# Kernel optimization log

Measured on AMD Instinct MI355X. Metric: run time of the kernel, lower is better.

Reference implementation:

```python
import jax, jax.numpy as jnp
import numpy as np
import math

DIM_V = 512
NUM_HEADS = 8
LN_EPS = 1e-5


def _layer_norm(x, g, b):
    mu = jnp.mean(x, axis=-1, keepdims=True)
    var = jnp.mean(jnp.square(x - mu), axis=-1, keepdims=True)
    return (x - mu) * jax.lax.rsqrt(var + LN_EPS) * g + b


def setup_inputs() -> dict:
    key = jax.random.key(0)
    ks = jax.random.split(key, 12)
    B, Nq, Nk, Dq, Dk, Dv = 16, 1024, 1024, 512, 512, DIM_V
    s_q = 1.0 / math.sqrt(Dq)
    s_k = 1.0 / math.sqrt(Dk)
    s_v = 1.0 / math.sqrt(Dv)
    return {
        "Q": jax.random.normal(ks[0], (B, Nq, Dq), jnp.float32),
        "K": jax.random.normal(ks[1], (B, Nk, Dk), jnp.float32),
        "Wq": jax.random.normal(ks[2], (Dq, Dv), jnp.float32) * s_q,
        "bq": jnp.zeros((Dv,), jnp.float32),
        "Wk": jax.random.normal(ks[3], (Dk, Dv), jnp.float32) * s_k,
        "bk": jnp.zeros((Dv,), jnp.float32),
        "Wv": jax.random.normal(ks[4], (Dk, Dv), jnp.float32) * s_k,
        "bv": jnp.zeros((Dv,), jnp.float32),
        "Wo": jax.random.normal(ks[5], (Dv, Dv), jnp.float32) * s_v,
        "bo": jnp.zeros((Dv,), jnp.float32),
        "g0": jnp.ones((Dv,), jnp.float32),
        "b0": jnp.zeros((Dv,), jnp.float32),
        "g1": jnp.ones((Dv,), jnp.float32),
        "b1": jnp.zeros((Dv,), jnp.float32),
    }


def reference(Q, K, Wq, bq, Wk, bk, Wv, bv, Wo, bo, g0, b0, g1, b1):
    B, Nq, _ = Q.shape
    H = NUM_HEADS
    hd = DIM_V // H
    Qp = Q @ Wq + bq            # [B, Nq, Dv]
    Kp = K @ Wk + bk            # [B, Nk, Dv]
    Vp = K @ Wv + bv            # [B, Nk, Dv]
    # split heads: [B, N, H, hd]
    Qh = Qp.reshape(B, Nq, H, hd)
    Kh = Kp.reshape(B, -1, H, hd)
    Vh = Vp.reshape(B, -1, H, hd)
    # NOTE: original scales by sqrt(dim_V), not sqrt(head_dim)
    scores = jnp.einsum("bqhd,bkhd->bhqk", Qh, Kh) / math.sqrt(DIM_V)
    A = jax.nn.softmax(scores, axis=-1)          # [B, H, Nq, Nk]
    Oh = Qh + jnp.einsum("bhqk,bkhd->bqhd", A, Vh)  # residual on projected Q
    O = Oh.reshape(B, Nq, DIM_V)
    O = _layer_norm(O, g0, b0)
    O = O + jax.nn.relu(O @ Wo + bo)
    O = _layer_norm(O, g1, b1)
    return O
```

## Files before the change

### kernel.cpp

```cpp
#include <hip/hip_runtime.h>
#include <hip/hip_bf16.h>

typedef float f32x4 __attribute__((ext_vector_type(4)));
typedef float f32x16 __attribute__((ext_vector_type(16)));
typedef __bf16 bf16x8 __attribute__((ext_vector_type(8)));
typedef __bf16 bf16x4 __attribute__((ext_vector_type(4)));

#define MFMA(a, b, c) __builtin_amdgcn_mfma_f32_16x16x32_bf16(a, b, c, 0, 0, 0)
#define MFMA32(a, b, c) __builtin_amdgcn_mfma_f32_32x32x16_bf16(a, b, c, 0, 0, 0)
#define AS1 __attribute__((address_space(1)))
#define AS3 __attribute__((address_space(3)))

__device__ __forceinline__ void gload16(const void* g, void* l) {
    __builtin_amdgcn_global_load_lds((const AS1 unsigned int*)g, (AS3 unsigned int*)l, 16, 0, 0);
}

__device__ __forceinline__ unsigned short f2bf(float f) {
    union { float f; unsigned u; } x{f};
    unsigned r = x.u + 0x7FFFu + ((x.u >> 16) & 1u);
    return (unsigned short)(r >> 16);
}
__device__ __forceinline__ float bf2f(unsigned short u) {
    union { unsigned u; float f; } x; x.u = ((unsigned)u) << 16; return x.f;
}
__device__ __forceinline__ unsigned pkbf(float a, float b) {
    union { __bf16 h[2]; unsigned u; } r;
    r.h[0] = (__bf16)a; r.h[1] = (__bf16)b;
    return r.u;
}

__device__ __forceinline__ void softmax_pack(const f32x16& s0, const f32x16& s1,
                                             float& ls, int hi, bf16x8* pf) {
    unsigned We[8], Wf[8];
    #pragma unroll
    for (int g = 0; g < 4; ++g) {
        float e0 = __builtin_amdgcn_exp2f(s0[4 * g + 0]);
        float e1 = __builtin_amdgcn_exp2f(s0[4 * g + 1]);
        float e2 = __builtin_amdgcn_exp2f(s0[4 * g + 2]);
        float e3 = __builtin_amdgcn_exp2f(s0[4 * g + 3]);
        float f0 = __builtin_amdgcn_exp2f(s1[4 * g + 0]);
        float f1 = __builtin_amdgcn_exp2f(s1[4 * g + 1]);
        float f2 = __builtin_amdgcn_exp2f(s1[4 * g + 2]);
        float f3 = __builtin_amdgcn_exp2f(s1[4 * g + 3]);
        ls += ((e0 + e1) + (e2 + e3)) + ((f0 + f1) + (f2 + f3));
        We[2 * g + 0] = pkbf(e0, e1); We[2 * g + 1] = pkbf(e2, e3);
        Wf[2 * g + 0] = pkbf(f0, f1); Wf[2 * g + 1] = pkbf(f2, f3);
    }
    #pragma unroll
    for (int src = 0; src < 2; ++src) {
        const unsigned* W = src == 0 ? We : Wf;
        #pragma unroll
        for (int k2 = 0; k2 < 2; ++k2) {
            unsigned A0 = W[4 * k2 + 0], A1 = W[4 * k2 + 1];
            unsigned B0 = W[4 * k2 + 2], B1 = W[4 * k2 + 3];
            unsigned cross0 = __shfl_xor(hi ? A0 : B0, 32);
            unsigned cross1 = __shfl_xor(hi ? A1 : B1, 32);
            union { unsigned w[4]; bf16x8 v; } r;
            r.w[0] = hi ? cross0 : A0;
            r.w[1] = hi ? cross1 : A1;
            r.w[2] = hi ? B0 : cross0;
            r.w[3] = hi ? B1 : cross1;
            pf[src * 2 + k2] = r.v;
        }
    }
}

__global__ __launch_bounds__(256) void k_transpose4(const float* W0, const float* W1,
                                                    const float* W2, const float* W3,
                                                    unsigned short* T0, unsigned short* T1,
                                                    unsigned short* T2, unsigned short* T3) {
    __shared__ float T[64][65];
    int sel = blockIdx.x >> 6, tile = blockIdx.x & 63;
    const float* W = sel == 0 ? W0 : sel == 1 ? W1 : sel == 2 ? W2 : W3;
    unsigned short* Wt = sel == 0 ? T0 : sel == 1 ? T1 : sel == 2 ? T2 : T3;
    int k0 = (tile >> 3) * 64, n0 = (tile & 7) * 64;
    int tid = threadIdx.x;
    for (int it = 0; it < 16; ++it) {
        int id = it * 256 + tid;
        int r = id >> 6, c = id & 63;
        T[r][c] = W[(k0 + r) * 512 + n0 + c];
    }
    __syncthreads();
    for (int it = 0; it < 16; ++it) {
        int id = it * 256 + tid;
        int r = id >> 6, c = id & 63;
        Wt[(n0 + r) * 512 + k0 + c] = f2bf(T[c][r]);
    }
}

__global__ __launch_bounds__(256) void k_proj(const float* __restrict__ Qf,
                                              const float* __restrict__ Kf,
                                              const unsigned short* __restrict__ Wqt,
                                              const unsigned short* __restrict__ Wkt,
                                              const unsigned short* __restrict__ Wvt,
                                              const float* __restrict__ bq,
                                              const float* __restrict__ bk,
                                              const float* __restrict__ bv,
                                              unsigned short* __restrict__ Qsc,
                                              unsigned short* __restrict__ Kpo,
                                              unsigned short* __restrict__ VpT,
                                              float scale2) {
    __shared__ __align__(16) float AbS[2][4096];
    __shared__ __align__(16) unsigned short BbS[2][4096];
    const int tid = threadIdx.x;
    const int lane = tid & 63, w = tid >> 6;
    const int sel = blockIdx.x >> 9;
    int ib = blockIdx.x & 511;
    const float* A = sel == 0 ? Qf : Kf;
    const unsigned short* Bt = sel == 0 ? Wqt : sel == 1 ? Wkt : Wvt;
    const float* bias = sel == 0 ? bq : sel == 1 ? bk : bv;
    const float scale = sel == 0 ? scale2 : 1.0f;
    const int mt = (ib & 7) | ((ib >> 5) << 3), nt = (ib >> 3) & 3;
    const int m0 = mt * 128, n0 = nt * 128;
    const int wm = (w >> 1) * 64, wn = (w & 1) * 64;
    const int l15 = lane & 15, l4 = lane >> 4;

    const f32x4 vz = {0.f, 0.f, 0.f, 0.f};
    f32x4 acc[4][4];
    for (int i = 0; i < 4; ++i)
        for (int j = 0; j < 4; ++j) acc[i][j] = vz;

    const float* Abase = A + (size_t)m0 * 512;
    const unsigned short* Bbase = Bt + (size_t)n0 * 512;

    auto STAGE = [&](int ks, int p) {
        int kk = ks * 32;
        #pragma unroll
        for (int it = 0; it < 4; ++it) {
            int id = it * 256 + tid;
            int r = id >> 3, cc = id & 7, g = cc ^ (r & 7);
            gload16(Abase + r * 512 + kk + g * 4, &AbS[p][(it * 256 + w * 64) * 4]);
        }
        #pragma unroll
        for (int it = 0; it < 2; ++it) {
            int id = it * 256 + tid;
            int r = id >> 2, x = id & 3, c = x ^ (r & 3);
            gload16(Bbase + r * 512 + kk + c * 8, &BbS[p][(it * 256 + w * 64) * 8]);
        }
    };

    STAGE(0, 0);
    __syncthreads();
    for (int ks = 0; ks < 16; ++ks) {
        int p = ks & 1;
        if (ks < 15) STAGE(ks + 1, p ^ 1);
        bf16x8 af[4], bfr[4];
        #pragma unroll
        for (int i = 0; i < 4; ++i) {
            int r = wm + i * 16 + l15;
            int pc0 = (2 * l4) ^ (r & 7);
            const float* Af = &AbS[p][r * 32];
            f32x4 a0 = *(const f32x4*)(Af + pc0 * 4);
            f32x4 a1 = *(const f32x4*)(Af + (pc0 ^ 1) * 4);
            af[i] = bf16x8{(__bf16)a0[0], (__bf16)a0[1], (__bf16)a0[2], (__bf16)a0[3],
                           (__bf16)a1[0], (__bf16)a1[1], (__bf16)a1[2], (__bf16)a1[3]};
        }
        #pragma unroll
        for (int j = 0; j < 4; ++j) {
            int r = wn + j * 16 + l15, pc = l4 ^ (r & 3);
            bfr[j] = *(const bf16x8*)&BbS[p][r * 32 + pc * 8];
        }
        __builtin_amdgcn_s_setprio(1);
        #pragma unroll
        for (int i = 0; i < 4; ++i)
            #pragma unroll
            for (int j = 0; j < 4; ++j)
                acc[i][j] = MFMA(af[i], bfr[j], acc[i][j]);
        __builtin_amdgcn_s_setprio(0);
        __syncthreads();
    }

    float bn[4];
    for (int j = 0; j < 4; ++j) bn[j] = bias[n0 + wn + j * 16 + l15];

    if (sel < 2) {
        unsigned short* out = sel == 0 ? Qsc : Kpo;
        for (int i = 0; i < 4; ++i)
            for (int j = 0; j < 4; ++j)
                for (int rg = 0; rg < 4; ++rg) {
                    int m = m0 + wm + i * 16 + l4 * 4 + rg;
                    int n = n0 + wn + j * 16 + l15;
                    out[(size_t)m * 512 + n] = f2bf((acc[i][j][rg] + bn[j]) * scale);
                }
    } else {
        unsigned short* T = (unsigned short*)&AbS[0][0] + w * 4096;
        __syncthreads();
        for (int i = 0; i < 4; ++i)
            for (int j = 0; j < 4; ++j)
                for (int rg = 0; rg < 4; ++rg) {
                    int ml = i * 16 + l4 * 4 + rg;
                    int nl = j * 16 + l15;
                    int pc = (ml >> 3) ^ (nl & 7);
                    T[nl * 64 + pc * 8 + (ml & 7)] = f2bf(acc[i][j][rg] + bn[j]);
                }
        int b = (m0 + wm) >> 10;
        int key0 = (m0 + wm) & 1023;
        for (int it = 0; it < 8; ++it) {
            int ch = it * 64 + lane;
            int nl = ch >> 3, c = ch & 7, pc = c ^ (nl & 7);
            int4 v = *(const int4*)&T[nl * 64 + pc * 8];
            int d = n0 + wn + nl;
            *(int4*)(VpT + ((size_t)b * 512 + d) * 1024 + key0 + c * 8) = v;
        }
    }
}

__global__ __launch_bounds__(128, 2) void k_attn64(const unsigned short* __restrict__ Qs,
                                                   const unsigned short* __restrict__ Kp,
                                                   const unsigned short* __restrict__ VpT,
                                                   unsigned short* __restrict__ O1b) {
    __shared__ __align__(16) unsigned short sm[16384];
    const int tid = threadIdx.x, lane = tid & 63, w = tid >> 6;
    const int l31 = lane & 31, hi = lane >> 5;
    int i = blockIdx.x;
    const int xcd = i & 7, r2 = i >> 3;
    const int bhl = r2 & 15, qt = r2 >> 4;
    const int bh = xcd * 16 + bhl;
    const int h = bh & 7, b = bh >> 3;
    const int q0 = b * 1024 + qt * 128 + w * 64;
    const int kv0 = (qt * 3 + bhl * 5) & 15;

    const unsigned short* Ksrc = Kp + (size_t)(b * 1024) * 512 + h * 64;
    const unsigned short* Vsrc = VpT + (size_t)(b * 512 + h * 64) * 1024;
    const unsigned short* qptrA = Qs + (size_t)(q0 + l31) * 512 + h * 64;
    const unsigned short* qptrB = qptrA + (size_t)32 * 512;

    bf16x8 qfA[4], qfB[4];
    #pragma unroll
    for (int ks = 0; ks < 4; ++ks) {
        qfA[ks] = *(const bf16x8*)(qptrA + ks * 16 + hi * 8);
        qfB[ks] = *(const bf16x8*)(qptrB + ks * 16 + hi * 8);
    }

    f32x16 accA0, accA1, accB0, accB1;
    #pragma unroll
    for (int r = 0; r < 16; ++r) { accA0[r] = 0.f; accA1[r] = 0.f; accB0[r] = 0.f; accB1[r] = 0.f; }
    float lsA = 0.f, lsB = 0.f;

    auto STAGE = [&](int j, int p) {
        int t = (j + kv0) & 15;
        #pragma unroll
        for (int it = 0; it < 4; ++it) {
            int id = it * 128 + tid;
            int r = id >> 3, x = id & 7, c = x ^ (r & 7);
            unsigned short* kb = sm + p * 4096 + (it * 128 + w * 64) * 8;
            gload16(Ksrc + (size_t)(t * 64 + r) * 512 + c * 8, kb);
            gload16(Vsrc + (size_t)r * 1024 + t * 64 + c * 8, kb + 8192);
        }
    };

    STAGE(0, 0);
    __syncthreads();
    const int rsw = l31 & 7;
    for (int it2 = 0; it2 < 16; ++it2) {
        int p = it2 & 1;
        if (it2 < 15) STAGE(it2 + 1, p ^ 1);
        const unsigned short* Kl = sm + p * 4096;
        const unsigned short* Vl = sm + 8192 + p * 4096;

        f32x16 s0a, s1a, s0b, s1b;
        #pragma unroll
        for (int r = 0; r < 16; ++r) { s0a[r] = 0.f; s1a[r] = 0.f; s0b[r] = 0.f; s1b[r] = 0.f; }
        __builtin_amdgcn_s_setprio(1);
        #pragma unroll
        for (int ks = 0; ks < 4; ++ks) {
            int c = (2 * ks + hi) ^ rsw;
            bf16x8 kf0 = *(const bf16x8*)&Kl[l31 * 64 + c * 8];
            bf16x8 kf1 = *(const bf16x8*)&Kl[(32 + l31) * 64 + c * 8];
            s0a = MFMA32(kf0, qfA[ks], s0a);
            s1a = MFMA32(kf1, qfA[ks], s1a);
            s0b = MFMA32(kf0, qfB[ks], s0b);
            s1b = MFMA32(kf1, qfB[ks], s1b);
        }
        __builtin_amdgcn_s_setprio(0);

        bf16x8 pfA[4], pfB[4];
        softmax_pack(s0a, s1a, lsA, hi, pfA);
        softmax_pack(s0b, s1b, lsB, hi, pfB);

        __builtin_amdgcn_s_setprio(1);
        #pragma unroll
        for (int ks = 0; ks < 4; ++ks) {
            int c = (2 * ks + hi) ^ rsw;
            bf16x8 vf0 = *(const bf16x8*)&Vl[l31 * 64 + c * 8];
            bf16x8 vf1 = *(const bf16x8*)&Vl[(32 + l31) * 64 + c * 8];
            accA0 = MFMA32(vf0, pfA[ks], accA0);
            accA1 = MFMA32(vf1, pfA[ks], accA1);
            accB0 = MFMA32(vf0, pfB[ks], accB0);
            accB1 = MFMA32(vf1, pfB[ks], accB1);
        }
        __builtin_amdgcn_s_setprio(0);
        __syncthreads();
    }

    const float invscale = 15.6841306f;
    {
        float l = lsA + __shfl_xor(lsA, 32);
        float linv = 1.0f / l;
        unsigned short* orow = O1b + (size_t)(q0 + l31) * 512 + h * 64;
        #pragma unroll
        for (int g = 0; g < 4; ++g) {
            int d0 = 8 * g + 4 * hi;
            bf16x4 qres = *(const bf16x4*)(qptrA + d0);
            bf16x4 ov;
            for (int j = 0; j < 4; ++j)
                ov[j] = (__bf16)((float)qres[j] * invscale + accA0[4 * g + j] * linv);
            *(bf16x4*)(orow + d0) = ov;
            int d1 = 32 + d0;
            bf16x4 qres1 = *(const bf16x4*)(qptrA + d1);
            bf16x4 ov1;
            for (int j = 0; j < 4; ++j)
                ov1[j] = (__bf16)((float)qres1[j] * invscale + accA1[4 * g + j] * linv);
            *(bf16x4*)(orow + d1) = ov1;
        }
    }
    {
        float l = lsB + __shfl_xor(lsB, 32);
        float linv = 1.0f / l;
        unsigned short* orow = O1b + (size_t)(q0 + 32 + l31) * 512 + h * 64;
        #pragma unroll
        for (int g = 0; g < 4; ++g) {
            int d0 = 8 * g + 4 * hi;
            bf16x4 qres = *(const bf16x4*)(qptrB + d0);
            bf16x4 ov;
            for (int j = 0; j < 4; ++j)
                ov[j] = (__bf16)((float)qres[j] * invscale + accB0[4 * g + j] * linv);
            *(bf16x4*)(orow + d0) = ov;
            int d1 = 32 + d0;
            bf16x4 qres1 = *(const bf16x4*)(qptrB + d1);
            bf16x4 ov1;
            for (int j = 0; j < 4; ++j)
                ov1[j] = (__bf16)((float)qres1[j] * invscale + accB1[4 * g + j] * linv);
            *(bf16x4*)(orow + d1) = ov1;
        }
    }
}

__global__ __launch_bounds__(256) void k_ln_bf(const unsigned short* __restrict__ in,
                                               unsigned short* __restrict__ outb,
                                               const float* __restrict__ g,
                                               const float* __restrict__ bt) {
    int row = blockIdx.x * 4 + (threadIdx.x >> 6);
    int lane = threadIdx.x & 63;
    const unsigned short* x = in + (size_t)row * 512 + lane * 8;
    bf16x8 v = *(const bf16x8*)x;
    float f[8];
    for (int j = 0; j < 8; ++j) f[j] = (float)v[j];
    float s1 = 0.f, s2 = 0.f;
    for (int j = 0; j < 8; ++j) { s1 += f[j]; s2 += f[j] * f[j]; }
    for (int off = 32; off; off >>= 1) {
        s1 += __shfl_xor(s1, off);
        s2 += __shfl_xor(s2, off);
    }
    float mu = s1 * (1.f / 512.f);
    float var = s2 * (1.f / 512.f) - mu * mu;
    float rs = rsqrtf(var + 1e-5f);
    float4 ga = *(const float4*)(g + lane * 8), gb = *(const float4*)(g + lane * 8 + 4);
    float4 ba = *(const float4*)(bt + lane * 8), bb = *(const float4*)(bt + lane * 8 + 4);
    float gg[8] = {ga.x, ga.y, ga.z, ga.w, gb.x, gb.y, gb.z, gb.w};
    float bv[8] = {ba.x, ba.y, ba.z, ba.w, bb.x, bb.y, bb.z, bb.w};
    bf16x8 y;
    for (int j = 0; j < 8; ++j) y[j] = (__bf16)((f[j] - mu) * rs * gg[j] + bv[j]);
    *(bf16x8*)(outb + (size_t)row * 512 + lane * 8) = y;
}

__global__ __launch_bounds__(512, 2) void k_gemm2ln(const unsigned short* __restrict__ A,
                                                    const unsigned short* __restrict__ Bt,
                                                    const float* __restrict__ bias,
                                                    const float* __restrict__ g1,
                                                    const float* __restrict__ b1,
                                                    float* __restrict__ out) {
    __shared__ __align__(16) unsigned short Ab[2][2048];
    __shared__ __align__(16) unsigned short Bb[2][16384];
    __shared__ float part[64][4][2];
    __shared__ float stats[64][2];
    const int tid = threadIdx.x, lane = tid & 63, w = tid >> 6;
    const int l15 = lane & 15, l4 = lane >> 4;
    const int m0 = blockIdx.x * 64;
    const int wm = (w >> 2) * 32, wn = (w & 3) * 128;

    const f32x4 vz = {0.f, 0.f, 0.f, 0.f};
    f32x4 acc[2][8];
    for (int i = 0; i < 2; ++i)
        for (int j = 0; j < 8; ++j) acc[i][j] = vz;

    const unsigned short* Abase = A + (size_t)m0 * 512;

    auto STAGE = [&](int ks, int p) {
        int kk = ks * 32;
        for (int it = 0; it < 4; ++it) {
            int id = it * 512 + tid;
            int r = id >> 2, x = id & 3, c = x ^ (r & 3);
            gload16(Bt + r * 512 + kk + c * 8, &Bb[p][(it * 512 + w * 64) * 8]);
        }
        if (w < 4) {
            int id = w * 64 + lane;
            int r = id >> 2, x = id & 3, c = x ^ (r & 3);
            gload16(Abase + r * 512 + kk + c * 8, &Ab[p][(w * 64) * 8]);
        }
    };

    STAGE(0, 0);
    __syncthreads();
    for (int ks = 0; ks < 16; ++ks) {
        int p = ks & 1;
        if (ks < 15) STAGE(ks + 1, p ^ 1);
        bf16x8 af[2], bfr[8];
        for (int i = 0; i < 2; ++i) {
            int r = wm + i * 16 + l15, pc = l4 ^ (r & 3);
            af[i] = *(const bf16x8*)&Ab[p][r * 32 + pc * 8];
        }
        for (int j = 0; j < 8; ++j) {
            int r = wn + j * 16 + l15, pc = l4 ^ (r & 3);
            bfr[j] = *(const bf16x8*)&Bb[p][r * 32 + pc * 8];
        }
        __builtin_amdgcn_s_setprio(1);
        for (int i = 0; i < 2; ++i)
            for (int j = 0; j < 8; ++j)
                acc[i][j] = MFMA(af[i], bfr[j], acc[i][j]);
        __builtin_amdgcn_s_setprio(0);
        __syncthreads();
    }

    float bn[8], gv[8], bv2[8];
    for (int j = 0; j < 8; ++j) {
        int n = wn + j * 16 + l15;
        bn[j] = bias[n]; gv[j] = g1[n]; bv2[j] = b1[n];
    }
    f32x4 s1v[2], s2v[2];
    for (int i = 0; i < 2; ++i) { s1v[i] = vz; s2v[i] = vz; }
    for (int i = 0; i < 2; ++i)
        for (int j = 0; j < 8; ++j)
            for (int rg = 0; rg < 4; ++rg) {
                int row = m0 + wm + i * 16 + l4 * 4 + rg;
                int n = wn + j * 16 + l15;
                float z = acc[i][j][rg] + bn[j];
                z = z > 0.f ? z : 0.f;
                float v = bf2f(A[(size_t)row * 512 + n]) + z;
                acc[i][j][rg] = v;
                s1v[i][rg] += v;
                s2v[i][rg] += v * v;
            }
    for (int i = 0; i < 2; ++i)
        for (int rg = 0; rg < 4; ++rg) {
            float a = s1v[i][rg], c = s2v[i][rg];
            for (int off = 1; off < 16; off <<= 1) {
                a += __shfl_xor(a, off);
                c += __shfl_xor(c, off);
            }
            s1v[i][rg] = a; s2v[i][rg] = c;
        }
    if (l15 == 0)
        for (int i = 0; i < 2; ++i)
            for (int rg = 0; rg < 4; ++rg) {
                int rl = wm + i * 16 + l4 * 4 + rg;
                part[rl][w & 3][0] = s1v[i][rg];
                part[rl][w & 3][1] = s2v[i][rg];
            }
    __syncthreads();
    if (tid < 64) {
        float a = 0.f, c = 0.f;
        for (int q = 0; q < 4; ++q) { a += part[tid][q][0]; c += part[tid][q][1]; }
        float mu = a * (1.f / 512.f);
        float var = c * (1.f / 512.f) - mu * mu;
        stats[tid][0] = mu;
        stats[tid][1] = rsqrtf(var + 1e-5f);
    }
    __syncthreads();
    for (int i = 0; i < 2; ++i)
        for (int rg = 0; rg < 4; ++rg) {
            int rl = wm + i * 16 + l4 * 4 + rg;
            float mu = stats[rl][0], rs = stats[rl][1];
            for (int j = 0; j < 8; ++j) {
                int n = wn + j * 16 + l15;
                out[(size_t)(m0 + rl) * 512 + n] = (acc[i][j][rg] - mu) * rs * gv[j] + bv2[j];
            }
        }
}

extern "C" void kernel_launch(void* const* d_in, const int* in_sizes, int n_in,
                              void* d_out, int out_size, void* d_ws, size_t ws_size,
                              hipStream_t stream) {
    const float* Q  = (const float*)d_in[0];
    const float* K  = (const float*)d_in[1];
    const float* Wq = (const float*)d_in[2];
    const float* bq = (const float*)d_in[3];
    const float* Wk = (const float*)d_in[4];
    const float* bk = (const float*)d_in[5];
    const float* Wv = (const float*)d_in[6];
    const float* bv = (const float*)d_in[7];
    const float* Wo = (const float*)d_in[8];
    const float* bo = (const float*)d_in[9];
    const float* g0 = (const float*)d_in[10];
    const float* b0 = (const float*)d_in[11];
    const float* g1 = (const float*)d_in[12];
    const float* b1 = (const float*)d_in[13];
    float* out = (float*)d_out;

    const size_t SZ_BF = (size_t)16384 * 512 * 2;
    const size_t SZ_W  = (size_t)512 * 512 * 2;
    char* p = (char*)d_ws;
    unsigned short* Wqt = (unsigned short*)p; p += SZ_W;
    unsigned short* Wkt = (unsigned short*)p; p += SZ_W;
    unsigned short* Wvt = (unsigned short*)p; p += SZ_W;
    unsigned short* Wot = (unsigned short*)p; p += SZ_W;
    unsigned short* Qsc = (unsigned short*)p; p += SZ_BF;
    unsigned short* Kp  = (unsigned short*)p; p += SZ_BF;
    unsigned short* VpT = (unsigned short*)p; p += SZ_BF;
    unsigned short* A1b = (unsigned short*)p; p += SZ_BF;
    unsigned short* X0b = (unsigned short*)p; p += SZ_BF;

    k_transpose4<<<256, 256, 0, stream>>>(Wq, Wk, Wv, Wo, Wqt, Wkt, Wvt, Wot);

    const float scale2 = 0.063758718f;
    k_proj<<<1536, 256, 0, stream>>>(Q, K, Wqt, Wkt, Wvt, bq, bk, bv, Qsc, Kp, VpT, scale2);

    k_attn64<<<1024, 128, 0, stream>>>(Qsc, Kp, VpT, A1b);

    k_ln_bf<<<4096, 256, 0, stream>>>(A1b, X0b, g0, b0);
    k_gemm2ln<<<256, 512, 0, stream>>>(X0b, Wot, bo, g1, b1, out);
}
```

Measured before the change: 142.5 us.

## Restructure QKV projection with MFMA-packed weights read directly from global

The Q/K/V weights are pre-packed into MFMA fragment order, so projection kernels load B fragments straight from global/L2 without LDS staging. The A operand is converted to bf16 once when written to LDS instead of on every fragment read. Each block now covers 64 rows by the full 512 columns with 8 waves, so every A tile is read once. The V projection becomes its own kernel that swaps MFMA operands to write the transposed output directly, with no LDS transpose. The trade-off is heavier global weight traffic per block, strided scalar VpT stores, and an extra kernel launch.

```diff
diff --git a/kernel.cpp b/kernel.cpp
--- a/kernel.cpp
+++ b/kernel.cpp
@@ -65,14 +65,14 @@
     }
 }
 
-__global__ __launch_bounds__(256) void k_transpose4(const float* W0, const float* W1,
-                                                    const float* W2, const float* W3,
-                                                    unsigned short* T0, unsigned short* T1,
-                                                    unsigned short* T2, unsigned short* T3) {
+__global__ __launch_bounds__(256) void k_pack4(const float* W0, const float* W1,
+                                               const float* W2, const float* W3,
+                                               unsigned short* P0, unsigned short* P1,
+                                               unsigned short* P2, unsigned short* P3) {
     __shared__ float T[64][65];
     int sel = blockIdx.x >> 6, tile = blockIdx.x & 63;
     const float* W = sel == 0 ? W0 : sel == 1 ? W1 : sel == 2 ? W2 : W3;
-    unsigned short* Wt = sel == 0 ? T0 : sel == 1 ? T1 : sel == 2 ? T2 : T3;
+    unsigned short* Wp = sel == 0 ? P0 : sel == 1 ? P1 : sel == 2 ? P2 : P3;
     int k0 = (tile >> 3) * 64, n0 = (tile & 7) * 64;
     int tid = threadIdx.x;
     for (int it = 0; it < 16; ++it) {
@@ -81,127 +81,178 @@
         T[r][c] = W[(k0 + r) * 512 + n0 + c];
     }
     __syncthreads();
-    for (int it = 0; it < 16; ++it) {
-        int id = it * 256 + tid;
-        int r = id >> 6, c = id & 63;
-        Wt[(n0 + r) * 512 + k0 + c] = f2bf(T[c][r]);
-    }
-}
-
-__global__ __launch_bounds__(256) void k_proj(const float* __restrict__ Qf,
-                                              const float* __restrict__ Kf,
-                                              const unsigned short* __restrict__ Wqt,
-                                              const unsigned short* __restrict__ Wkt,
-                                              const unsigned short* __restrict__ Wvt,
-                                              const float* __restrict__ bq,
-                                              const float* __restrict__ bk,
-                                              const float* __restrict__ bv,
-                                              unsigned short* __restrict__ Qsc,
-                                              unsigned short* __restrict__ Kpo,
-                                              unsigned short* __restrict__ VpT,
-                                              float scale2) {
-    __shared__ __align__(16) float AbS[2][4096];
-    __shared__ __align__(16) unsigned short BbS[2][4096];
-    const int tid = threadIdx.x;
-    const int lane = tid & 63, w = tid >> 6;
-    const int sel = blockIdx.x >> 9;
-    int ib = blockIdx.x & 511;
-    const float* A = sel == 0 ? Qf : Kf;
-    const unsigned short* Bt = sel == 0 ? Wqt : sel == 1 ? Wkt : Wvt;
-    const float* bias = sel == 0 ? bq : sel == 1 ? bk : bv;
-    const float scale = sel == 0 ? scale2 : 1.0f;
-    const int mt = (ib & 7) | ((ib >> 5) << 3), nt = (ib >> 3) & 3;
-    const int m0 = mt * 128, n0 = nt * 128;
-    const int wm = (w >> 1) * 64, wn = (w & 1) * 64;
+    if (sel < 3) {
+        #pragma unroll
+        for (int cc = 0; cc < 2; ++cc) {
+            int ch = cc * 256 + tid;
+            int ksl = ch >> 8, n16l = (ch >> 6) & 3, ln = ch & 63;
+            int kg = ln >> 4, nl = ln & 15;
+            union { unsigned short u[8]; int4 v; } tmp;
+            #pragma unroll
+            for (int e = 0; e < 8; ++e)
+                tmp.u[e] = f2bf(T[ksl * 32 + kg * 8 + e][n16l * 16 + nl]);
+            size_t dst = ((size_t)((k0 >> 5) + ksl) * 32 + (n0 >> 4) + n16l) * 512 + ln * 8;
+            *(int4*)(Wp + dst) = tmp.v;
+        }
+    } else {
+        for (int it = 0; it < 16; ++it) {
+            int id = it * 256 + tid;
+            int r = id >> 6, c = id & 63;
+            Wp[(n0 + r) * 512 + k0 + c] = f2bf(T[c][r]);
+        }
+    }
+}
+
+__global__ __launch_bounds__(512, 4) void k_projQK(const float* __restrict__ Qf,
+                                                   const float* __restrict__ Kf,
+                                                   const unsigned short* __restrict__ WpQ,
+                                                   const unsigned short* __restrict__ WpK,
+                                                   const float* __restrict__ bq,
+                                                   const float* __restrict__ bk,
+                                                   unsigned short* __restrict__ Qsc,
+                                                   unsigned short* __restrict__ Kp,
+                                                   float scale2) {
+    __shared__ __align__(16) unsigned short Asm[2][2048];
+    const int tid = threadIdx.x, lane = tid & 63, w = tid >> 6;
     const int l15 = lane & 15, l4 = lane >> 4;
+    const int bid = blockIdx.x;
+    const int sel = bid >> 8, rt = bid & 255;
+    const float* A = sel ? Kf : Qf;
+    const unsigned short* Wp = sel ? WpK : WpQ;
+    const float* bias = sel ? bk : bq;
+    unsigned short* out = sel ? Kp : Qsc;
+    const float scale = sel ? 1.0f : scale2;
+    const int m0 = rt * 64;
+    const int wn = w * 64;
 
     const f32x4 vz = {0.f, 0.f, 0.f, 0.f};
     f32x4 acc[4][4];
     for (int i = 0; i < 4; ++i)
         for (int j = 0; j < 4; ++j) acc[i][j] = vz;
 
-    const float* Abase = A + (size_t)m0 * 512;
-    const unsigned short* Bbase = Bt + (size_t)n0 * 512;
-
-    auto STAGE = [&](int ks, int p) {
-        int kk = ks * 32;
-        #pragma unroll
-        for (int it = 0; it < 4; ++it) {
-            int id = it * 256 + tid;
-            int r = id >> 3, cc = id & 7, g = cc ^ (r & 7);
-            gload16(Abase + r * 512 + kk + g * 4, &AbS[p][(it * 256 + w * 64) * 4]);
-        }
-        #pragma unroll
-        for (int it = 0; it < 2; ++it) {
-            int id = it * 256 + tid;
-            int r = id >> 2, x = id & 3, c = x ^ (r & 3);
-            gload16(Bbase + r * 512 + kk + c * 8, &BbS[p][(it * 256 + w * 64) * 8]);
-        }
+    const int sr = tid >> 3, sc4 = tid & 7;
+    const float* aptr = A + (size_t)(m0 + sr) * 512 + sc4 * 4;
+    unsigned short* const wdst =
+        &Asm[0][0] + sr * 32 + ((sc4 >> 1) ^ (sr & 3)) * 8 + (sc4 & 1) * 4;
+
+    auto WRITEA = [&](const float4& v, int p) {
+        union { unsigned u[2]; } r;
+        r.u[0] = pkbf(v.x, v.y);
+        r.u[1] = pkbf(v.z, v.w);
+        *(uint2*)(wdst + p * 2048) = *(uint2*)&r;
     };
 
-    STAGE(0, 0);
-    __syncthreads();
+    {
+        float4 a0 = *(const float4*)(aptr);
+        WRITEA(a0, 0);
+    }
+    __syncthreads();
+
+    const unsigned short* wbase = Wp + (size_t)(w * 4) * 512 + lane * 8;
     for (int ks = 0; ks < 16; ++ks) {
         int p = ks & 1;
-        if (ks < 15) STAGE(ks + 1, p ^ 1);
-        bf16x8 af[4], bfr[4];
+        float4 anx;
+        if (ks < 15) anx = *(const float4*)(aptr + (ks + 1) * 32);
+        bf16x8 bfr[4], afr[4];
+        #pragma unroll
+        for (int j = 0; j < 4; ++j)
+            bfr[j] = *(const bf16x8*)(wbase + (size_t)ks * 16384 + j * 512);
         #pragma unroll
         for (int i = 0; i < 4; ++i) {
-            int r = wm + i * 16 + l15;
-            int pc0 = (2 * l4) ^ (r & 7);
-            const float* Af = &AbS[p][r * 32];
-            f32x4 a0 = *(const f32x4*)(Af + pc0 * 4);
-            f32x4 a1 = *(const f32x4*)(Af + (pc0 ^ 1) * 4);
-            af[i] = bf16x8{(__bf16)a0[0], (__bf16)a0[1], (__bf16)a0[2], (__bf16)a0[3],
-                           (__bf16)a1[0], (__bf16)a1[1], (__bf16)a1[2], (__bf16)a1[3]};
-        }
-        #pragma unroll
-        for (int j = 0; j < 4; ++j) {
-            int r = wn + j * 16 + l15, pc = l4 ^ (r & 3);
-            bfr[j] = *(const bf16x8*)&BbS[p][r * 32 + pc * 8];
+            int rr = i * 16 + l15;
+            afr[i] = *(const bf16x8*)&Asm[p][rr * 32 + (l4 ^ (rr & 3)) * 8];
         }
         __builtin_amdgcn_s_setprio(1);
         #pragma unroll
         for (int i = 0; i < 4; ++i)
             #pragma unroll
             for (int j = 0; j < 4; ++j)
-                acc[i][j] = MFMA(af[i], bfr[j], acc[i][j]);
+                acc[i][j] = MFMA(afr[i], bfr[j], acc[i][j]);
         __builtin_amdgcn_s_setprio(0);
+        if (ks < 15) WRITEA(anx, p ^ 1);
         __syncthreads();
     }
 
     float bn[4];
-    for (int j = 0; j < 4; ++j) bn[j] = bias[n0 + wn + j * 16 + l15];
-
-    if (sel < 2) {
-        unsigned short* out = sel == 0 ? Qsc : Kpo;
+    #pragma unroll
+    for (int j = 0; j < 4; ++j) bn[j] = bias[wn + j * 16 + l15];
+    for (int i = 0; i < 4; ++i)
+        for (int j = 0; j < 4; ++j)
+            for (int rg = 0; rg < 4; ++rg) {
+                int m = m0 + i * 16 + l4 * 4 + rg;
+                int n = wn + j * 16 + l15;
+                out[(size_t)m * 512 + n] = f2bf((acc[i][j][rg] + bn[j]) * scale);
+            }
+}
+
+__global__ __launch_bounds__(512, 4) void k_projV(const float* __restrict__ Kf,
+                                                  const unsigned short* __restrict__ WpV,
+                                                  const float* __restrict__ bv,
+                                                  unsigned short* __restrict__ VpT) {
+    __shared__ __align__(16) unsigned short Asm[2][2048];
+    const int tid = threadIdx.x, lane = tid & 63, w = tid >> 6;
+    const int l15 = lane & 15, l4 = lane >> 4;
+    const int rt = blockIdx.x;
+    const int m0 = rt * 64;
+    const int wn = w * 64;
+
+    const f32x4 vz = {0.f, 0.f, 0.f, 0.f};
+    f32x4 acc[4][4];
+    for (int i = 0; i < 4; ++i)
+        for (int j = 0; j < 4; ++j) acc[i][j] = vz;
+
+    const int sr = tid >> 3, sc4 = tid & 7;
+    const float* aptr = Kf + (size_t)(m0 + sr) * 512 + sc4 * 4;
+    unsigned short* const wdst =
+        &Asm[0][0] + sr * 32 + ((sc4 >> 1) ^ (sr & 3)) * 8 + (sc4 & 1) * 4;
+
+    auto WRITEA = [&](const float4& v, int p) {
+        union { unsigned u[2]; } r;
+        r.u[0] = pkbf(v.x, v.y);
+        r.u[1] = pkbf(v.z, v.w);
+        *(uint2*)(wdst + p * 2048) = *(uint2*)&r;
+    };
+
+    {
+        float4 a0 = *(const float4*)(aptr);
+        WRITEA(a0, 0);
+    }
+    __syncthreads();
+
+    const unsigned short* wbase = WpV + (size_t)(w * 4) * 512 + lane * 8;
+    for (int ks = 0; ks < 16; ++ks) {
+        int p = ks & 1;
+        float4 anx;
+        if (ks < 15) anx = *(const float4*)(aptr + (ks + 1) * 32);
+        bf16x8 bfr[4], afr[4];
+        #pragma unroll
+        for (int j = 0; j < 4; ++j)
+            bfr[j] = *(const bf16x8*)(wbase + (size_t)ks * 16384 + j * 512);
+        #pragma unroll
+        for (int i = 0; i < 4; ++i) {
+            int rr = i * 16 + l15;
+            afr[i] = *(const bf16x8*)&Asm[p][rr * 32 + (l4 ^ (rr & 3)) * 8];
+        }
+        __builtin_amdgcn_s_setprio(1);
+        #pragma unroll
         for (int i = 0; i < 4; ++i)
+            #pragma unroll
             for (int j = 0; j < 4; ++j)
-                for (int rg = 0; rg < 4; ++rg) {
-                    int m = m0 + wm + i * 16 + l4 * 4 + rg;
-                    int n = n0 + wn + j * 16 + l15;
-                    out[(size_t)m * 512 + n] = f2bf((acc[i][j][rg] + bn[j]) * scale);
-                }
-    } else {
-        unsigned short* T = (unsigned short*)&AbS[0][0] + w * 4096;
+                acc[i][j] = MFMA(bfr[j], afr[i], acc[i][j]);
+        __builtin_amdgcn_s_setprio(0);
+        if (ks < 15) WRITEA(anx, p ^ 1);
         __syncthreads();
+    }
+
+    const int b = m0 >> 10, key0 = m0 & 1023;
+    for (int j = 0; j < 4; ++j) {
+        float4 bv4 = *(const float4*)(bv + wn + j * 16 + l4 * 4);
         for (int i = 0; i < 4; ++i)
-            for (int j = 0; j < 4; ++j)
-                for (int rg = 0; rg < 4; ++rg) {
-                    int ml = i * 16 + l4 * 4 + rg;
-                    int nl = j * 16 + l15;
-                    int pc = (ml >> 3) ^ (nl & 7);
-                    T[nl * 64 + pc * 8 + (ml & 7)] = f2bf(acc[i][j][rg] + bn[j]);
-                }
-        int b = (m0 + wm) >> 10;
-        int key0 = (m0 + wm) & 1023;
-        for (int it = 0; it < 8; ++it) {
-            int ch = it * 64 + lane;
-            int nl = ch >> 3, c = ch & 7, pc = c ^ (nl & 7);
-            int4 v = *(const int4*)&T[nl * 64 + pc * 8];
-            int d = n0 + wn + nl;
-            *(int4*)(VpT + ((size_t)b * 512 + d) * 1024 + key0 + c * 8) = v;
-        }
+            for (int rg = 0; rg < 4; ++rg) {
+                int d = wn + j * 16 + l4 * 4 + rg;
+                int key = key0 + i * 16 + l15;
+                VpT[((size_t)(b * 512 + d)) * 1024 + key] = f2bf(acc[i][j][rg] + bv4[rg]);
+            }
     }
 }
 
@@ -500,9 +551,9 @@
     const size_t SZ_BF = (size_t)16384 * 512 * 2;
     const size_t SZ_W  = (size_t)512 * 512 * 2;
     char* p = (char*)d_ws;
-    unsigned short* Wqt = (unsigned short*)p; p += SZ_W;
-    unsigned short* Wkt = (unsigned short*)p; p += SZ_W;
-    unsigned short* Wvt = (unsigned short*)p; p += SZ_W;
+    unsigned short* WpQ = (unsigned short*)p; p += SZ_W;
+    unsigned short* WpK = (unsigned short*)p; p += SZ_W;
+    unsigned short* WpV = (unsigned short*)p; p += SZ_W;
     unsigned short* Wot = (unsigned short*)p; p += SZ_W;
     unsigned short* Qsc = (unsigned short*)p; p += SZ_BF;
     unsigned short* Kp  = (unsigned short*)p; p += SZ_BF;
@@ -510,10 +561,11 @@
     unsigned short* A1b = (unsigned short*)p; p += SZ_BF;
     unsigned short* X0b = (unsigned short*)p; p += SZ_BF;
 
-    k_transpose4<<<256, 256, 0, stream>>>(Wq, Wk, Wv, Wo, Wqt, Wkt, Wvt, Wot);
+    k_pack4<<<256, 256, 0, stream>>>(Wq, Wk, Wv, Wo, WpQ, WpK, WpV, Wot);
 
     const float scale2 = 0.063758718f;
-    k_proj<<<1536, 256, 0, stream>>>(Q, K, Wqt, Wkt, Wvt, bq, bk, bv, Qsc, Kp, VpT, scale2);
+    k_projQK<<<512, 512, 0, stream>>>(Q, K, WpQ, WpK, bq, bk, Qsc, Kp, scale2);
+    k_projV<<<256, 512, 0, stream>>>(K, WpV, bv, VpT);
 
     k_attn64<<<1024, 128, 0, stream>>>(Qsc, Kp, VpT, A1b);
 
```

After: 145.5 us. +2.1%, slower.
